# Performance work log

Measured on AMD Instinct MI355X. Metric: run time of the kernel, lower is better.

The kernel has to match this reference:

```python
import jax, jax.numpy as jnp
import numpy as np

N, D, S, M = 32, 128, 128, 64
BASIS = 5


def setup_inputs() -> dict:
    key = jax.random.key(0)
    k1, k2 = jax.random.split(key)
    inputs = jax.random.normal(k1, (N, D, M, M), dtype=jnp.float32)
    coeffs = jax.random.normal(k2, (D, S, BASIS), dtype=jnp.float32) * np.sqrt(2.0) / (D + S)
    all_bias = jnp.zeros((1, S, 1, 1), dtype=jnp.float32)
    return {"inputs": inputs, "coeffs": coeffs, "all_bias": all_bias}


def reference(inputs, coeffs, all_bias):
    # inputs: [N, D, m, m]
    m = inputs.shape[3]
    diag_part = jnp.diagonal(inputs, axis1=2, axis2=3)          # [N, D, m]
    mean_diag = jnp.mean(diag_part, axis=2, keepdims=True)      # [N, D, 1]
    mean_cols = jnp.mean(inputs, axis=2)                        # [N, D, m]
    mean_all = jnp.mean(mean_cols, axis=2)                      # [N, D]

    op1 = (mean_cols[:, :, :, None] + mean_cols[:, :, None, :]) / 2   # [N, D, m, m]
    op2 = inputs
    op3 = (diag_part[:, :, :, None] + diag_part[:, :, None, :]) / 2
    op4 = jnp.broadcast_to(mean_diag[:, :, :, None], inputs.shape)
    op5 = jnp.broadcast_to(mean_all[:, :, None, None], inputs.shape)

    ops_out = jnp.stack([op1, op2, op3, op4, op5], axis=2)      # [N, D, 5, m, m]
    output = jnp.einsum('dsb,ndbij->nsij', coeffs, ops_out)     # [N, S, m, m]
    return output + all_bias
```

## Files before the change

### kernel.cpp

```cpp
#include <hip/hip_runtime.h>

#define NN 32
#define DD 128
#define SS 128
#define MM 64
#define PP 4096
#define DSZ (DD * SS)

typedef short bf16x8 __attribute__((ext_vector_type(8)));
typedef float f32x4  __attribute__((ext_vector_type(4)));

#define OFF_CPK 0
#define OFF_C1T (OFF_CPK + 5 * DSZ)
#define OFF_MC  (OFF_C1T + DSZ / 2)
#define OFF_DG  (OFF_MC + NN * DD * MM)
#define OFF_MD  (OFF_DG + NN * DD * MM)
#define OFF_MA  (OFF_MD + NN * DD)
#define OFF_UP  (OFF_MA + NN * DD)

__device__ __forceinline__ unsigned int fbits(float f) {
    union { float f; unsigned int u; } c; c.f = f; return c.u;
}

__global__ __launch_bounds__(256) void pack_k(const float* __restrict__ coeffs,
                                              float* __restrict__ cpk,
                                              unsigned short* __restrict__ c1t) {
    int g = blockIdx.x * 256 + threadIdx.x;
    int d = g >> 7, s = g & 127;
    float v0 = coeffs[g * 5 + 0];
    float v1 = coeffs[g * 5 + 1];
    float v2 = coeffs[g * 5 + 2];
    float v3 = coeffs[g * 5 + 3];
    float v4 = coeffs[g * 5 + 4];
    cpk[0 * DSZ + g] = v0;
    cpk[2 * DSZ + g] = v2;
    cpk[3 * DSZ + g] = v3;
    cpk[4 * DSZ + g] = v4;
    unsigned int u = fbits(v1);
    u += 0x7fffu + ((u >> 16) & 1);
    c1t[s * DD + d] = (unsigned short)(u >> 16);
}

__global__ __launch_bounds__(256) void stats_k(const float* __restrict__ x,
                                               float* __restrict__ mc,
                                               float* __restrict__ dg,
                                               float* __restrict__ md,
                                               float* __restrict__ ma) {
    int nd = blockIdx.x * 4 + (threadIdx.x >> 6);
    int l  = threadIdx.x & 63;
    const float* base = x + (size_t)nd * PP;
    int iq = l >> 4, jq = l & 15;

    float4 cs = make_float4(0.f, 0.f, 0.f, 0.f);
    float dv = 0.f;
#pragma unroll
    for (int r = 0; r < 16; ++r) {
        float4 v = *(const float4*)(base + (r * 4 + iq) * MM + jq * 4);
        cs.x += v.x; cs.y += v.y; cs.z += v.z; cs.w += v.w;
        if (r == jq)
            dv = (iq == 0) ? v.x : (iq == 1) ? v.y : (iq == 2) ? v.z : v.w;
    }
#pragma unroll
    for (int m = 16; m <= 32; m <<= 1) {
        cs.x += __shfl_xor(cs.x, m);
        cs.y += __shfl_xor(cs.y, m);
        cs.z += __shfl_xor(cs.z, m);
        cs.w += __shfl_xor(cs.w, m);
    }
    if (iq == 0) {
        float4 o = make_float4(cs.x * (1.f / 64.f), cs.y * (1.f / 64.f),
                               cs.z * (1.f / 64.f), cs.w * (1.f / 64.f));
        *(float4*)(mc + nd * MM + jq * 4) = o;
    }
    dg[nd * MM + 4 * jq + iq] = dv;
    float dsum = dv;
#pragma unroll
    for (int m = 1; m <= 32; m <<= 1) dsum += __shfl_xor(dsum, m);
    float tot = cs.x + cs.y + cs.z + cs.w;
#pragma unroll
    for (int m = 1; m <= 8; m <<= 1) tot += __shfl_xor(tot, m);
    if (l == 0) {
        md[nd] = dsum * (1.f / 64.f);
        ma[nd] = tot * (1.f / 4096.f);
    }
}

__global__ __launch_bounds__(256) void combine_k(const float* __restrict__ cpk,
                                                 const float* __restrict__ mc,
                                                 const float* __restrict__ dg,
                                                 const float* __restrict__ md,
                                                 const float* __restrict__ ma,
                                                 const float* __restrict__ bias,
                                                 float* __restrict__ up) {
    int sg = blockIdx.x, n = blockIdx.y;
    int t  = threadIdx.x;
    int i  = t & 63;
    int sq = t >> 6;
    int s0 = sg * 16 + sq * 4;

    const float* c0p = cpk + 0 * DSZ;
    const float* c2p = cpk + 2 * DSZ;
    const float* c3p = cpk + 3 * DSZ;
    const float* c4p = cpk + 4 * DSZ;

    float wacc[4] = {0.f, 0.f, 0.f, 0.f};
    float vacc[4] = {0.f, 0.f, 0.f, 0.f};
#pragma unroll 2
    for (int d = 0; d < DD; ++d) {
        int bidx = (n * DD + d) * MM + i;
        float m  = mc[bidx];
        float g  = dg[bidx];
        float mdv = md[n * DD + d];
        float mav = ma[n * DD + d];
#pragma unroll
        for (int r = 0; r < 4; ++r) {
            int cs = d * SS + s0 + r;
            wacc[r] += c0p[cs] * m + c2p[cs] * g;
            vacc[r] += c3p[cs] * mdv + c4p[cs] * mav;
        }
    }
#pragma unroll
    for (int r = 0; r < 4; ++r) {
        int s = s0 + r;
        up[((size_t)n * SS + s) * MM + i] = 0.5f * (wacc[r] + vacc[r] + bias[s]);
    }
}

#define USTR 68
__global__ __launch_bounds__(256, 3) void gemm_k(const float* __restrict__ x,
                                                 const unsigned short* __restrict__ c1t,
                                                 const float* __restrict__ up,
                                                 float* __restrict__ out) {
    __shared__ float us[SS * USTR];

    int n  = blockIdx.y;
    int p0 = blockIdx.x * 128;
    int t  = threadIdx.x;
    int w  = t >> 6, l = t & 63;
    int wp = w & 1, wsn = w >> 1;
    int q  = l >> 4, c = l & 15;

    const float* upn = up + (size_t)n * SS * MM;
#pragma unroll
    for (int e = t; e < SS * MM / 4; e += 256) {
        int s  = e >> 4;
        int i4 = (e & 15) * 4;
        *(f32x4*)&us[s * USTR + i4] = *(const f32x4*)(upn + s * MM + i4);
    }
    __syncthreads();

    int p0w = p0 + wp * 64;
    int s0w = wsn * 64;
    int iw  = p0w >> 6;
    const float* xb = x + (size_t)n * DD * PP;

    f32x4 acc[4][4];
#pragma unroll
    for (int a = 0; a < 4; ++a)
#pragma unroll
        for (int b = 0; b < 4; ++b) acc[a][b] = (f32x4)0.f;

#pragma unroll
    for (int kt = 0; kt < 4; ++kt) {
        int k0 = kt * 32 + q * 8;
        bf16x8 af[4];
#pragma unroll
        for (int st = 0; st < 4; ++st)
            af[st] = *(const bf16x8*)(c1t + (size_t)(s0w + st * 16 + c) * DD + k0);
#pragma unroll
        for (int pt = 0; pt < 4; ++pt) {
            const float* xp = xb + (size_t)k0 * PP + (p0w + pt * 16 + c);
            float f0 = xp[0 * PP], f1 = xp[1 * PP], f2 = xp[2 * PP], f3 = xp[3 * PP];
            float f4 = xp[4 * PP], f5 = xp[5 * PP], f6 = xp[6 * PP], f7 = xp[7 * PP];
            union { unsigned int u[4]; bf16x8 v; } bb;
            bb.u[0] = __builtin_amdgcn_perm(fbits(f1), fbits(f0), 0x07060302u);
            bb.u[1] = __builtin_amdgcn_perm(fbits(f3), fbits(f2), 0x07060302u);
            bb.u[2] = __builtin_amdgcn_perm(fbits(f5), fbits(f4), 0x07060302u);
            bb.u[3] = __builtin_amdgcn_perm(fbits(f7), fbits(f6), 0x07060302u);
#pragma unroll
            for (int st = 0; st < 4; ++st)
                acc[st][pt] = __builtin_amdgcn_mfma_f32_16x16x32_bf16(af[st], bb.v,
                                                                     acc[st][pt], 0, 0, 0);
        }
    }

#pragma unroll
    for (int st = 0; st < 4; ++st) {
#pragma unroll
        for (int r = 0; r < 4; ++r) {
            int s = s0w + st * 16 + q * 4 + r;
            float uiv = us[s * USTR + iw];
            float* orow = out + ((size_t)(n * SS + s)) * PP;
#pragma unroll
            for (int pt = 0; pt < 4; ++pt) {
                int p = p0w + pt * 16 + c;
                int j = p & 63;
                orow[p] = acc[st][pt][r] + uiv + us[s * USTR + j];
            }
        }
    }
}

extern "C" void kernel_launch(void* const* d_in, const int* in_sizes, int n_in,
                              void* d_out, int out_size, void* d_ws, size_t ws_size,
                              hipStream_t stream) {
    const float* x      = (const float*)d_in[0];
    const float* coeffs = (const float*)d_in[1];
    const float* bias   = (const float*)d_in[2];
    float* out = (float*)d_out;
    float* ws  = (float*)d_ws;

    float*          cpk = ws + OFF_CPK;
    unsigned short* c1t = (unsigned short*)(ws + OFF_C1T);
    float*          mc  = ws + OFF_MC;
    float*          dg  = ws + OFF_DG;
    float*          md  = ws + OFF_MD;
    float*          ma  = ws + OFF_MA;
    float*          up  = ws + OFF_UP;

    pack_k<<<DSZ / 256, 256, 0, stream>>>(coeffs, cpk, c1t);
    stats_k<<<NN * DD / 4, 256, 0, stream>>>(x, mc, dg, md, ma);
    combine_k<<<dim3(8, NN), 256, 0, stream>>>(cpk, mc, dg, md, ma, bias, up);
    gemm_k<<<dim3(PP / 128, NN), 256, 0, stream>>>(x, c1t, up, out);
}
```

Measured before the change: 171.2 us.

## Fold coefficient packing into stats kernel and re-layout combine output as [n,i,s]

```diff
diff --git a/kernel.cpp b/kernel.cpp
--- a/kernel.cpp
+++ b/kernel.cpp
@@ -10,9 +10,9 @@
 typedef short bf16x8 __attribute__((ext_vector_type(8)));
 typedef float f32x4  __attribute__((ext_vector_type(4)));
 
-#define OFF_CPK 0
-#define OFF_C1T (OFF_CPK + 5 * DSZ)
-#define OFF_MC  (OFF_C1T + DSZ / 2)
+#define OFF_C1T 0
+#define OFF_CPL (OFF_C1T + DSZ / 2)
+#define OFF_MC  (OFF_CPL + 4 * DSZ)
 #define OFF_DG  (OFF_MC + NN * DD * MM)
 #define OFF_MD  (OFF_DG + NN * DD * MM)
 #define OFF_MA  (OFF_MD + NN * DD)
@@ -22,30 +22,28 @@
     union { float f; unsigned int u; } c; c.f = f; return c.u;
 }
 
-__global__ __launch_bounds__(256) void pack_k(const float* __restrict__ coeffs,
-                                              float* __restrict__ cpk,
-                                              unsigned short* __restrict__ c1t) {
-    int g = blockIdx.x * 256 + threadIdx.x;
-    int d = g >> 7, s = g & 127;
-    float v0 = coeffs[g * 5 + 0];
-    float v1 = coeffs[g * 5 + 1];
-    float v2 = coeffs[g * 5 + 2];
-    float v3 = coeffs[g * 5 + 3];
-    float v4 = coeffs[g * 5 + 4];
-    cpk[0 * DSZ + g] = v0;
-    cpk[2 * DSZ + g] = v2;
-    cpk[3 * DSZ + g] = v3;
-    cpk[4 * DSZ + g] = v4;
-    unsigned int u = fbits(v1);
-    u += 0x7fffu + ((u >> 16) & 1);
-    c1t[s * DD + d] = (unsigned short)(u >> 16);
-}
-
 __global__ __launch_bounds__(256) void stats_k(const float* __restrict__ x,
+                                               const float* __restrict__ coeffs,
                                                float* __restrict__ mc,
                                                float* __restrict__ dg,
                                                float* __restrict__ md,
-                                               float* __restrict__ ma) {
+                                               float* __restrict__ ma,
+                                               float* __restrict__ cpl,
+                                               unsigned short* __restrict__ c1t) {
+    if (blockIdx.x < 64) {
+        int gd = blockIdx.x * 256 + threadIdx.x;
+        const float* cp = coeffs + (size_t)gd * 5;
+        float4 v03 = *(const float4*)cp;
+        float  v4  = cp[4];
+        cpl[0 * DSZ + gd] = v03.x;
+        cpl[1 * DSZ + gd] = v03.z;
+        cpl[2 * DSZ + gd] = v03.w;
+        cpl[3 * DSZ + gd] = v4;
+        unsigned int u = fbits(v03.y);
+        u += 0x7fffu + ((u >> 16) & 1);
+        c1t[(gd & 127) * DD + (gd >> 7)] = (unsigned short)(u >> 16);
+    }
+
     int nd = blockIdx.x * 4 + (threadIdx.x >> 6);
     int l  = threadIdx.x & 63;
     const float* base = x + (size_t)nd * PP;
@@ -85,53 +83,41 @@
     }
 }
 
-__global__ __launch_bounds__(256) void combine_k(const float* __restrict__ cpk,
+__global__ __launch_bounds__(128) void combine_k(const float* __restrict__ cpl,
                                                  const float* __restrict__ mc,
                                                  const float* __restrict__ dg,
                                                  const float* __restrict__ md,
                                                  const float* __restrict__ ma,
                                                  const float* __restrict__ bias,
                                                  float* __restrict__ up) {
-    int sg = blockIdx.x, n = blockIdx.y;
-    int t  = threadIdx.x;
-    int i  = t & 63;
-    int sq = t >> 6;
-    int s0 = sg * 16 + sq * 4;
-
-    const float* c0p = cpk + 0 * DSZ;
-    const float* c2p = cpk + 2 * DSZ;
-    const float* c3p = cpk + 3 * DSZ;
-    const float* c4p = cpk + 4 * DSZ;
-
-    float wacc[4] = {0.f, 0.f, 0.f, 0.f};
-    float vacc[4] = {0.f, 0.f, 0.f, 0.f};
-#pragma unroll 2
+    int i = blockIdx.x;
+    int n = blockIdx.y;
+    int s = threadIdx.x;
+
+    const float* c0p = cpl + 0 * DSZ + s;
+    const float* c2p = cpl + 1 * DSZ + s;
+    const float* c3p = cpl + 2 * DSZ + s;
+    const float* c4p = cpl + 3 * DSZ + s;
+
+    float w = 0.f, v = 0.f;
+#pragma unroll 4
     for (int d = 0; d < DD; ++d) {
-        int bidx = (n * DD + d) * MM + i;
-        float m  = mc[bidx];
-        float g  = dg[bidx];
+        float mcv = mc[(n * DD + d) * MM + i];
+        float dgv = dg[(n * DD + d) * MM + i];
         float mdv = md[n * DD + d];
         float mav = ma[n * DD + d];
-#pragma unroll
-        for (int r = 0; r < 4; ++r) {
-            int cs = d * SS + s0 + r;
-            wacc[r] += c0p[cs] * m + c2p[cs] * g;
-            vacc[r] += c3p[cs] * mdv + c4p[cs] * mav;
-        }
-    }
-#pragma unroll
-    for (int r = 0; r < 4; ++r) {
-        int s = s0 + r;
-        up[((size_t)n * SS + s) * MM + i] = 0.5f * (wacc[r] + vacc[r] + bias[s]);
-    }
-}
-
-#define USTR 68
+        w += c0p[d * SS] * mcv + c2p[d * SS] * dgv;
+        v += c3p[d * SS] * mdv + c4p[d * SS] * mav;
+    }
+    up[((size_t)n * MM + i) * SS + s] = 0.5f * (w + v + bias[s]);
+}
+
+#define SSTR 129
 __global__ __launch_bounds__(256, 3) void gemm_k(const float* __restrict__ x,
                                                  const unsigned short* __restrict__ c1t,
                                                  const float* __restrict__ up,
                                                  float* __restrict__ out) {
-    __shared__ float us[SS * USTR];
+    __shared__ float us[MM * SSTR];
 
     int n  = blockIdx.y;
     int p0 = blockIdx.x * 128;
@@ -140,12 +126,16 @@
     int wp = w & 1, wsn = w >> 1;
     int q  = l >> 4, c = l & 15;
 
-    const float* upn = up + (size_t)n * SS * MM;
-#pragma unroll
-    for (int e = t; e < SS * MM / 4; e += 256) {
-        int s  = e >> 4;
-        int i4 = (e & 15) * 4;
-        *(f32x4*)&us[s * USTR + i4] = *(const f32x4*)(upn + s * MM + i4);
+    const float* upn = up + (size_t)n * MM * SS;
+#pragma unroll
+    for (int e = t; e < MM * SS / 4; e += 256) {
+        int i  = e >> 5;
+        int s4 = (e & 31) * 4;
+        f32x4 vv = *(const f32x4*)(upn + i * SS + s4);
+        us[i * SSTR + s4 + 0] = vv.x;
+        us[i * SSTR + s4 + 1] = vv.y;
+        us[i * SSTR + s4 + 2] = vv.z;
+        us[i * SSTR + s4 + 3] = vv.w;
     }
     __syncthreads();
 
@@ -189,13 +179,13 @@
 #pragma unroll
         for (int r = 0; r < 4; ++r) {
             int s = s0w + st * 16 + q * 4 + r;
-            float uiv = us[s * USTR + iw];
+            float uiv = us[iw * SSTR + s];
             float* orow = out + ((size_t)(n * SS + s)) * PP;
 #pragma unroll
             for (int pt = 0; pt < 4; ++pt) {
                 int p = p0w + pt * 16 + c;
                 int j = p & 63;
-                orow[p] = acc[st][pt][r] + uiv + us[s * USTR + j];
+                orow[p] = acc[st][pt][r] + uiv + us[j * SSTR + s];
             }
         }
     }
@@ -210,16 +200,15 @@
     float* out = (float*)d_out;
     float* ws  = (float*)d_ws;
 
-    float*          cpk = ws + OFF_CPK;
     unsigned short* c1t = (unsigned short*)(ws + OFF_C1T);
+    float*          cpl = ws + OFF_CPL;
     float*          mc  = ws + OFF_MC;
     float*          dg  = ws + OFF_DG;
     float*          md  = ws + OFF_MD;
     float*          ma  = ws + OFF_MA;
     float*          up  = ws + OFF_UP;
 
-    pack_k<<<DSZ / 256, 256, 0, stream>>>(coeffs, cpk, c1t);
-    stats_k<<<NN * DD / 4, 256, 0, stream>>>(x, mc, dg, md, ma);
-    combine_k<<<dim3(8, NN), 256, 0, stream>>>(cpk, mc, dg, md, ma, bias, up);
+    stats_k<<<NN * DD / 4, 256, 0, stream>>>(x, coeffs, mc, dg, md, ma, cpl, c1t);
+    combine_k<<<dim3(MM, NN), 128, 0, stream>>>(cpl, mc, dg, md, ma, bias, up);
     gemm_k<<<dim3(PP / 128, NN), 256, 0, stream>>>(x, c1t, up, out);
 }
```

Measured after the change: 175.4 us. 1.02x slower.
